# Optimization experiments

Hardware: AMD Instinct MI355X
Metric: run time of the kernel (lower is better)

Reference implementation:

```python
import jax, jax.numpy as jnp
import numpy as np
import math

DIM = 1024
NUM_HEADS = 16
QUANTUM_HEADS = 2
HEAD_DIM = DIM // NUM_HEADS          # 64
TRAD_HEADS = NUM_HEADS - QUANTUM_HEADS  # 14
B, S = 1, 1024
STEPS = 2048
LN_EPS = 1e-5


def setup_inputs() -> dict:
    key = jax.random.key(0)
    ks = jax.random.split(key, 10)
    hd2 = 2 * HEAD_DIM
    return {
        "x": jax.random.normal(ks[0], (B, S, DIM), jnp.float32),
        # to_quantum_state: Linear(head_dim -> 2*head_dim) + LayerNorm + Tanh (shared across quantum heads)
        "qs_W": jax.random.normal(ks[1], (hd2, HEAD_DIM), jnp.float32) / math.sqrt(HEAD_DIM),
        "qs_b": jnp.zeros((hd2,), jnp.float32),
        "ln_g": jnp.ones((hd2,), jnp.float32),
        "ln_b": jnp.zeros((hd2,), jnp.float32),
        # per-quantum-head scalars
        "q_freq": jax.random.normal(ks[2], (QUANTUM_HEADS,), jnp.float32) * 0.02,
        "q_shift": jax.random.normal(ks[3], (QUANTUM_HEADS,), jnp.float32) * 0.02,
        # traditional head projections (no bias)
        "Wq": jax.random.normal(ks[4], (TRAD_HEADS * HEAD_DIM, DIM), jnp.float32) / math.sqrt(DIM),
        "Wk": jax.random.normal(ks[5], (TRAD_HEADS * HEAD_DIM, DIM), jnp.float32) / math.sqrt(DIM),
        "Wv": jax.random.normal(ks[6], (TRAD_HEADS * HEAD_DIM, DIM), jnp.float32) / math.sqrt(DIM),
        # output projection (with bias)
        "Wo": jax.random.normal(ks[7], (DIM, DIM), jnp.float32) / math.sqrt(DIM),
        "bo": jnp.zeros((DIM,), jnp.float32),
    }


def _layernorm(h, g, b):
    mu = jnp.mean(h, axis=-1, keepdims=True)
    var = jnp.mean(jnp.square(h - mu), axis=-1, keepdims=True)
    return (h - mu) * jax.lax.rsqrt(var + LN_EPS) * g + b


def _forward(x, qs_W, qs_b, ln_g, ln_b, q_freq, q_shift, Wq, Wk, Wv, Wo, bo):
    cos_table = jnp.cos(jnp.linspace(0.0, 2.0 * math.pi, STEPS).astype(jnp.float32))
    scale = 1.0 / math.sqrt(HEAD_DIM)
    two_pi = 2.0 * math.pi

    outs = []
    # ---- quantum heads (small fixed loop over structurally distinct heads) ----
    for h in range(QUANTUM_HEADS):
        xh = x[..., h * HEAD_DIM:(h + 1) * HEAD_DIM]          # (B,S,hd)
        qs = jnp.tanh(_layernorm(xh @ qs_W.T + qs_b, ln_g, ln_b))  # (B,S,2hd)
        amp, phase = jnp.split(qs, 2, axis=-1)                 # each (B,S,hd)
        # per (query pos i, key pos j, feature d) phase difference
        pd = (phase[:, :, None, :] - phase[:, None, :, :]) * q_freq[h] + q_shift[h]  # (B,S,S,hd)
        idx = jnp.floor(jnp.mod(pd / two_pi * STEPS, STEPS)).astype(jnp.int32)
        interf = cos_table[idx]                                # lookup-table gather, (B,S,S,hd)
        attn = jnp.einsum('bid,bjd,bijd->bij', amp, amp, interf) * scale
        attn = jax.nn.softmax(attn, axis=-1)
        outs.append(attn @ xh)                                 # (B,S,hd), values are the raw head slice

    # ---- traditional heads: standard multi-head attention ----
    q = (x @ Wq.T).reshape(B, S, TRAD_HEADS, HEAD_DIM)
    k = (x @ Wk.T).reshape(B, S, TRAD_HEADS, HEAD_DIM)
    v = (x @ Wv.T).reshape(B, S, TRAD_HEADS, HEAD_DIM)
    scores = jnp.einsum('bqhd,bkhd->bhqk', q, k) * scale       # (B,Ht,S,S)
    probs = jax.nn.softmax(scores, axis=-1)
    trad = jnp.einsum('bhqk,bkhd->bqhd', probs, v).reshape(B, S, TRAD_HEADS * HEAD_DIM)
    outs.append(trad)

    out = jnp.concatenate(outs, axis=-1)                       # (B,S,DIM)
    return out @ Wo.T + bo


def reference(x, qs_W, qs_b, ln_g, ln_b, q_freq, q_shift, Wq, Wk, Wv, Wo, bo):
    return _forward(x, qs_W, qs_b, ln_g, ln_b, q_freq, q_shift, Wq, Wk, Wv, Wo, bo)
```

## Files before the change

### kernel.cpp

```cpp
#include <hip/hip_runtime.h>
#include <hip/hip_bf16.h>
#include <math.h>

#define DIMX 1024
#define SEQ  1024
#define HD   64
#define QH   2
#define TH   14
#define QKVN 2688
#define LN_EPS 1e-5f
#define NB_F2B 4736
#define NB_QPREP 1024
#define NB_XT 32

typedef __bf16 bf16x8 __attribute__((ext_vector_type(8)));
typedef float  f32x4  __attribute__((ext_vector_type(4)));
typedef unsigned short u16x8 __attribute__((ext_vector_type(8)));

__device__ inline unsigned short f2b_rne(float f) {
  unsigned int u = __float_as_uint(f);
  unsigned int r = (u + 0x7FFF + ((u >> 16) & 1)) >> 16;
  return (unsigned short)r;
}

__device__ inline float waveRedSum(float v) {
  #pragma unroll
  for (int off = 32; off; off >>= 1) v += __shfl_xor(v, off, 64);
  return v;
}

__global__ __launch_bounds__(256) void k_prep(
    const float* __restrict__ x, const float* __restrict__ qsW,
    const float* __restrict__ qsb, const float* __restrict__ lng,
    const float* __restrict__ lnb, const float* __restrict__ qfreq,
    const float* __restrict__ qshift,
    const float* __restrict__ wq, const float* __restrict__ wk,
    const float* __restrict__ wv, const float* __restrict__ wo,
    unsigned short* __restrict__ x_bf, unsigned short* __restrict__ wqkv_bf,
    unsigned short* __restrict__ wo_bf,
    unsigned short* __restrict__ qcs, unsigned short* __restrict__ kcs,
    unsigned short* __restrict__ xt) {
  __shared__ float xrow2[2][HD];
  __shared__ float redm[2][2], redv[2][2];
  __shared__ float qsv2[2][128];
  __shared__ unsigned short ttile[64][72];
  int t = threadIdx.x;
  int bid = blockIdx.x;
  if (bid < NB_F2B) {
    long i = ((long)bid * 256 + t) * 4;
    float4 v;
    unsigned short* dst;
    if (i < 1048576) {
      v = *reinterpret_cast<const float4*>(x + i);
      dst = x_bf + i;
    } else if (i < 3801088) {
      long j = i - 1048576;
      const float* s = (j < 917504) ? wq + j
                     : (j < 1835008) ? wk + (j - 917504)
                                     : wv + (j - 1835008);
      v = *reinterpret_cast<const float4*>(s);
      dst = wqkv_bf + j;
    } else {
      long j = i - 3801088;
      v = *reinterpret_cast<const float4*>(wo + j);
      dst = wo_bf + j;
    }
    ushort4 o;
    o.x = f2b_rne(v.x); o.y = f2b_rne(v.y); o.z = f2b_rne(v.z); o.w = f2b_rne(v.w);
    *reinterpret_cast<ushort4*>(dst) = o;
  } else if (bid < NB_F2B + NB_QPREP) {
    int half = t >> 7, o = t & 127;
    int row = (bid - NB_F2B) * 2 + half;
    int h = row >> 10, i = row & 1023;
    if (o < HD) xrow2[half][o] = x[i * DIMX + h * HD + o];
    __syncthreads();
    float s = qsb[o];
    #pragma unroll
    for (int d = 0; d < HD; d += 4) {
      float4 w = *reinterpret_cast<const float4*>(qsW + o * HD + d);
      float4 xv = *reinterpret_cast<const float4*>(&xrow2[half][d]);
      s += xv.x * w.x + xv.y * w.y + xv.z * w.z + xv.w * w.w;
    }
    int wid = (o >> 6), lane = o & 63;
    float ws = waveRedSum(s);
    if (lane == 0) redm[half][wid] = ws;
    __syncthreads();
    float mu = (redm[half][0] + redm[half][1]) * (1.0f / 128.0f);
    float dv = s - mu;
    float ws2 = waveRedSum(dv * dv);
    if (lane == 0) redv[half][wid] = ws2;
    __syncthreads();
    float var = (redv[half][0] + redv[half][1]) * (1.0f / 128.0f);
    float y = dv * rsqrtf(var + LN_EPS) * lng[o] + lnb[o];
    qsv2[half][o] = tanhf(y);
    __syncthreads();
    float freq = qfreq[h], shift = qshift[h];
    size_t base = ((size_t)h * 1024 + i) * 128;
    if (o < HD) {
      float amp = qsv2[half][o];
      float a = qsv2[half][64 + o] * freq + shift;
      float sn, cs;
      __sincosf(a, &sn, &cs);
      qcs[base + o]      = f2b_rne(amp * cs);
      qcs[base + 64 + o] = f2b_rne(amp * sn);
    } else {
      int d = o - 64;
      float amp = qsv2[half][d];
      float bAng = qsv2[half][64 + d] * freq;
      float sn, cs;
      __sincosf(bAng, &sn, &cs);
      kcs[base + d]      = f2b_rne(amp * cs);
      kcs[base + 64 + d] = f2b_rne(amp * sn);
    }
  } else {
    int b = bid - (NB_F2B + NB_QPREP);
    int h = b >> 4, kv0 = (b & 15) * 64;
    #pragma unroll
    for (int pass = 0; pass < 2; ++pass) {
      int s = pass * 256 + t;
      int r = s >> 3, c8 = (s & 7) * 8;
      const float* src = x + (size_t)(kv0 + r) * DIMX + h * 64 + c8;
      float4 a = *reinterpret_cast<const float4*>(src);
      float4 b4 = *reinterpret_cast<const float4*>(src + 4);
      ushort4 o1, o2;
      o1.x = f2b_rne(a.x);  o1.y = f2b_rne(a.y);  o1.z = f2b_rne(a.z);  o1.w = f2b_rne(a.w);
      o2.x = f2b_rne(b4.x); o2.y = f2b_rne(b4.y); o2.z = f2b_rne(b4.z); o2.w = f2b_rne(b4.w);
      *reinterpret_cast<ushort4*>(&ttile[r][c8]) = o1;
      *reinterpret_cast<ushort4*>(&ttile[r][c8 + 4]) = o2;
    }
    __syncthreads();
    #pragma unroll
    for (int pass = 0; pass < 2; ++pass) {
      int s = pass * 256 + t;
      int d = s >> 3, k8 = (s & 7) * 8;
      u16x8 o;
      #pragma unroll
      for (int j = 0; j < 8; ++j) o[j] = ttile[k8 + j][d];
      *reinterpret_cast<u16x8*>(xt + (size_t)h * 65536 + (size_t)d * 1024 + kv0 + k8) = o;
    }
  }
}

template <int DQK, int NT>
__device__ __forceinline__ void dev_fattn(
    char* smem,
    const unsigned short* __restrict__ Qp, int ldq,
    const unsigned short* __restrict__ Kp, int ldk,
    const unsigned short* __restrict__ Vp,
    int q0, int split, int slot,
    float* __restrict__ pout, float* __restrict__ pml) {
  const int LQ = DQK + 8;
  const int KREG = DQK / 32;
  unsigned short* Qs  = (unsigned short*)smem;
  unsigned short* Ks0 = Qs + 64 * LQ;
  unsigned short* Ks1 = Ks0 + 64 * LQ;
  unsigned short* Vs0 = Ks1 + 64 * LQ;
  unsigned short* Vs1 = Vs0 + 64 * 72;
  unsigned short* Ps  = Vs1 + 64 * 72;
  int kv0 = split * (NT * 64);
  int t = threadIdx.x, lane = t & 63, w = t >> 6;
  int g = lane >> 4, li = lane & 15;

  #pragma unroll
  for (int i = 0; i < DQK / 32; ++i) {
    int s = i * 64 + lane;
    int r = s / (DQK / 8), c8 = (s % (DQK / 8)) * 8;
    u16x8 v = *reinterpret_cast<const u16x8*>(Qp + (size_t)(q0 + w * 16 + r) * ldq + c8);
    *reinterpret_cast<u16x8*>(&Qs[(w * 16 + r) * LQ + c8]) = v;
  }

  u16x8 kreg[KREG], vreg[2];
  auto loadKV = [&](int tile) {
    int j0 = kv0 + tile * 64;
    #pragma unroll
    for (int i = 0; i < KREG; ++i) {
      int s = i * 256 + t;
      int r = s / (DQK / 8), c8 = (s % (DQK / 8)) * 8;
      kreg[i] = *reinterpret_cast<const u16x8*>(Kp + (size_t)(j0 + r) * ldk + c8);
    }
    #pragma unroll
    for (int i = 0; i < 2; ++i) {
      int s = i * 256 + t;
      int d = s >> 3, c8 = (s & 7) * 8;
      vreg[i] = *reinterpret_cast<const u16x8*>(Vp + (size_t)d * 1024 + j0 + c8);
    }
  };
  auto writeKV = [&](int buf) {
    unsigned short* Ksb = buf ? Ks1 : Ks0;
    unsigned short* Vsb = buf ? Vs1 : Vs0;
    #pragma unroll
    for (int i = 0; i < KREG; ++i) {
      int s = i * 256 + t;
      int r = s / (DQK / 8), c8 = (s % (DQK / 8)) * 8;
      *reinterpret_cast<u16x8*>(&Ksb[r * LQ + c8]) = kreg[i];
    }
    #pragma unroll
    for (int i = 0; i < 2; ++i) {
      int s = i * 256 + t;
      int d = s >> 3, c8 = (s & 7) * 8;
      *reinterpret_cast<u16x8*>(&Vsb[d * 72 + c8]) = vreg[i];
    }
  };

  loadKV(0);
  writeKV(0);
  if (NT > 1) loadKV(1);
  __syncthreads();

  f32x4 acc_o[4] = {};
  float mrow[4] = {-1e30f, -1e30f, -1e30f, -1e30f};
  float lrow[4] = {0.f, 0.f, 0.f, 0.f};

  #pragma unroll
  for (int tile = 0; tile < NT; ++tile) {
    int cur = tile & 1;
    unsigned short* Ksc = cur ? Ks1 : Ks0;
    unsigned short* Vsc = cur ? Vs1 : Vs0;
    if (tile < NT - 1) writeKV(cur ^ 1);
    if (tile < NT - 2) loadKV(tile + 2);
    f32x4 s_acc[4] = {};
    #pragma unroll
    for (int kk = 0; kk < DQK / 32; ++kk) {
      bf16x8 aq = *reinterpret_cast<const bf16x8*>(&Qs[(w * 16 + li) * LQ + kk * 32 + g * 8]);
      #pragma unroll
      for (int n = 0; n < 4; ++n) {
        bf16x8 bk = *reinterpret_cast<const bf16x8*>(&Ksc[(n * 16 + li) * LQ + kk * 32 + g * 8]);
        s_acc[n] = __builtin_amdgcn_mfma_f32_16x16x32_bf16(aq, bk, s_acc[n], 0, 0, 0);
      }
    }
    #pragma unroll
    for (int r = 0; r < 4; ++r) {
      float tm = fmaxf(fmaxf(s_acc[0][r], s_acc[1][r]), fmaxf(s_acc[2][r], s_acc[3][r]));
      #pragma unroll
      for (int m = 1; m < 16; m <<= 1) tm = fmaxf(tm, __shfl_xor(tm, m, 64));
      float mn = fmaxf(mrow[r], tm);
      float sf = __expf((mrow[r] - mn) * 0.125f);
      mrow[r] = mn;
      lrow[r] *= sf;
      #pragma unroll
      for (int n = 0; n < 4; ++n) acc_o[n][r] *= sf;
      float rs = 0.f;
      #pragma unroll
      for (int n = 0; n < 4; ++n) {
        float p = __expf((s_acc[n][r] - mn) * 0.125f);
        s_acc[n][r] = p;
        rs += p;
      }
      #pragma unroll
      for (int m = 1; m < 16; m <<= 1) rs += __shfl_xor(rs, m, 64);
      lrow[r] += rs;
    }
    #pragma unroll
    for (int n = 0; n < 4; ++n)
      #pragma unroll
      for (int r = 0; r < 4; ++r)
        Ps[(w * 16 + g * 4 + r) * 72 + n * 16 + li] = f2b_rne(s_acc[n][r]);
    #pragma unroll
    for (int kk = 0; kk < 2; ++kk) {
      bf16x8 ap = *reinterpret_cast<const bf16x8*>(&Ps[(w * 16 + li) * 72 + kk * 32 + g * 8]);
      #pragma unroll
      for (int n = 0; n < 4; ++n) {
        bf16x8 bv = *reinterpret_cast<const bf16x8*>(&Vsc[(n * 16 + li) * 72 + kk * 32 + g * 8]);
        acc_o[n] = __builtin_amdgcn_mfma_f32_16x16x32_bf16(ap, bv, acc_o[n], 0, 0, 0);
      }
    }
    __syncthreads();
  }

  size_t rowbase = (size_t)slot * 1024;
  #pragma unroll
  for (int r = 0; r < 4; ++r) {
    int qr = q0 + w * 16 + g * 4 + r;
    #pragma unroll
    for (int n = 0; n < 4; ++n)
      pout[(rowbase + qr) * 64 + n * 16 + li] = acc_o[n][r];
    if (li == 0) {
      pml[(rowbase + qr) * 2 + 0] = mrow[r];
      pml[(rowbase + qr) * 2 + 1] = lrow[r];
    }
  }
}

__global__ __launch_bounds__(256) void k_fattn_all(
    const unsigned short* __restrict__ qcs, const unsigned short* __restrict__ kcs,
    const unsigned short* __restrict__ xt, const unsigned short* __restrict__ qkv,
    const unsigned short* __restrict__ vt,
    float* __restrict__ pout, float* __restrict__ pml) {
  __shared__ __align__(16) char smem[79872];
  int bid = blockIdx.x;
  if (bid < 256) {
    int qt = bid & 15, h = (bid >> 4) & 1, split = bid >> 5;
    dev_fattn<128, 2>(smem, qcs + (size_t)h * SEQ * 128, 128,
                      kcs + (size_t)h * SEQ * 128, 128,
                      xt + (size_t)h * 65536, qt * 64, split, h * 8 + split, pout, pml);
  } else {
    int b2 = bid - 256;
    int qt = b2 & 15, hs = b2 >> 4;
    int h = hs % 14, split = hs / 14;
    dev_fattn<64, 4>(smem, qkv + h * 64, QKVN,
                     qkv + 896 + h * 64, QKVN,
                     vt + (size_t)h * 65536, qt * 64, split, 16 + h * 4 + split, pout, pml);
  }
}

__global__ __launch_bounds__(256) void k_fmerge(
    const float* __restrict__ pout, const float* __restrict__ pml,
    unsigned short* __restrict__ concat) {
  int rq = blockIdx.x * 4 + (threadIdx.x >> 6);
  int lh = rq >> 10, q = rq & 1023;
  int d = threadIdx.x & 63;
  int s0 = (lh < 2) ? lh * 8 : 16 + (lh - 2) * 4;
  int ns = (lh < 2) ? 8 : 4;
  float m_s[8], l_s[8];
  float M = -1e30f;
  #pragma unroll
  for (int s = 0; s < 8; ++s) {
    if (s < ns) {
      size_t rb = (size_t)(s0 + s) * 1024 + q;
      m_s[s] = pml[rb * 2 + 0];
      l_s[s] = pml[rb * 2 + 1];
      M = fmaxf(M, m_s[s]);
    }
  }
  float num = 0.f, den = 0.f;
  #pragma unroll
  for (int s = 0; s < 8; ++s) {
    if (s < ns) {
      float wgt = __expf((m_s[s] - M) * 0.125f);
      num += wgt * pout[((size_t)(s0 + s) * 1024 + q) * 64 + d];
      den += wgt * l_s[s];
    }
  }
  concat[(size_t)q * DIMX + lh * 64 + d] = f2b_rne(num / den);
}

template <int HAS_BIAS, int BF16_OUT>
__global__ __launch_bounds__(256) void k_gemm64s(
    const unsigned short* __restrict__ A, const unsigned short* __restrict__ B,
    void* __restrict__ Cv, const float* __restrict__ bias,
    unsigned short* __restrict__ vtp,
    int K, int lda, int ldb, int ldc) {
  __shared__ unsigned short As[64 * 64];
  __shared__ unsigned short Bs[64 * 64];
  int t = threadIdx.x, lane = t & 63, w = t >> 6;
  int wr = w >> 1, wc = w & 1;
  int g = lane >> 4, li = lane & 15;
  int mb = blockIdx.y * 64, nb = blockIdx.x * 64;
  int rstg = t >> 3;
  int cswz = (((t & 7) ^ (rstg & 7)) * 8);
  f32x4 acc[2][2] = {};
  for (int kb = 0; kb < K; kb += 64) {
    __syncthreads();
    #pragma unroll
    for (int i = 0; i < 2; ++i) {
      __builtin_amdgcn_global_load_lds(
          (const __attribute__((address_space(1))) unsigned int*)(A + (size_t)(mb + i * 32 + rstg) * lda + kb + cswz),
          (__attribute__((address_space(3))) unsigned int*)(As + i * 2048 + t * 8), 16, 0, 0);
      __builtin_amdgcn_global_load_lds(
          (const __attribute__((address_space(1))) unsigned int*)(B + (size_t)(nb + i * 32 + rstg) * ldb + kb + cswz),
          (__attribute__((address_space(3))) unsigned int*)(Bs + i * 2048 + t * 8), 16, 0, 0);
    }
    __syncthreads();
    #pragma unroll
    for (int kk = 0; kk < 2; ++kk) {
      bf16x8 af[2], bfr[2];
      #pragma unroll
      for (int m = 0; m < 2; ++m) {
        int r = wr * 32 + m * 16 + li;
        int cb = kk * 4 + g;
        af[m] = *reinterpret_cast<const bf16x8*>(&As[r * 64 + ((cb ^ (r & 7)) * 8)]);
      }
      #pragma unroll
      for (int n = 0; n < 2; ++n) {
        int r = wc * 32 + n * 16 + li;
        int cb = kk * 4 + g;
        bfr[n] = *reinterpret_cast<const bf16x8*>(&Bs[r * 64 + ((cb ^ (r & 7)) * 8)]);
      }
      #pragma unroll
      for (int m = 0; m < 2; ++m)
        #pragma unroll
        for (int n = 0; n < 2; ++n)
          acc[m][n] = __builtin_amdgcn_mfma_f32_16x16x32_bf16(af[m], bfr[n], acc[m][n], 0, 0, 0);
    }
  }
  if (vtp != nullptr && nb >= 1792) {
    #pragma unroll
    for (int m = 0; m < 2; ++m) {
      int row0 = mb + wr * 32 + m * 16 + g * 4;
      #pragma unroll
      for (int n = 0; n < 2; ++n) {
        int colrel = nb - 1792 + wc * 32 + n * 16 + li;
        #pragma unroll
        for (int r = 0; r < 4; ++r)
          vtp[(size_t)colrel * 1024 + row0 + r] = f2b_rne(acc[m][n][r]);
      }
    }
    return;
  }
  #pragma unroll
  for (int m = 0; m < 2; ++m) {
    int row0 = mb + wr * 32 + m * 16 + g * 4;
    #pragma unroll
    for (int n = 0; n < 2; ++n) {
      int col = nb + wc * 32 + n * 16 + li;
      float bval = HAS_BIAS ? bias[col] : 0.0f;
      #pragma unroll
      for (int r = 0; r < 4; ++r) {
        size_t idx = (size_t)(row0 + r) * ldc + col;
        if (BF16_OUT) ((unsigned short*)Cv)[idx] = f2b_rne(acc[m][n][r] + bval);
        else          ((float*)Cv)[idx] = acc[m][n][r] + bval;
      }
    }
  }
}

extern "C" void kernel_launch(void* const* d_in, const int* in_sizes, int n_in,
                              void* d_out, int out_size, void* d_ws, size_t ws_size,
                              hipStream_t stream) {
  const float* x      = (const float*)d_in[0];
  const float* qsW    = (const float*)d_in[1];
  const float* qsb    = (const float*)d_in[2];
  const float* lng    = (const float*)d_in[3];
  const float* lnb    = (const float*)d_in[4];
  const float* qfreq  = (const float*)d_in[5];
  const float* qshift = (const float*)d_in[6];
  const float* Wq     = (const float*)d_in[7];
  const float* Wk     = (const float*)d_in[8];
  const float* Wv     = (const float*)d_in[9];
  const float* Wo     = (const float*)d_in[10];
  const float* bo     = (const float*)d_in[11];
  float* out = (float*)d_out;

  char* ws = (char*)d_ws;
  size_t off = 0;
  auto alloc = [&](size_t bytes) { char* p = ws + off; off += (bytes + 255) & ~(size_t)255; return p; };
  unsigned short* x_bf      = (unsigned short*)alloc((size_t)SEQ * DIMX * 2);
  unsigned short* wqkv_bf   = (unsigned short*)alloc((size_t)QKVN * DIMX * 2);
  unsigned short* wo_bf     = (unsigned short*)alloc((size_t)DIMX * DIMX * 2);
  unsigned short* concat_bf = (unsigned short*)alloc((size_t)SEQ * DIMX * 2);
  unsigned short* qkv_bf    = (unsigned short*)alloc((size_t)SEQ * QKVN * 2);
  unsigned short* qcs       = (unsigned short*)alloc((size_t)QH * SEQ * 128 * 2);
  unsigned short* kcs       = (unsigned short*)alloc((size_t)QH * SEQ * 128 * 2);
  unsigned short* vt        = (unsigned short*)alloc((size_t)TH * HD * SEQ * 2);
  unsigned short* xt        = (unsigned short*)alloc((size_t)QH * HD * SEQ * 2);
  float*          pout      = (float*)alloc((size_t)72 * SEQ * 64 * 4);
  float*          pml       = (float*)alloc((size_t)72 * SEQ * 2 * 4);

  k_prep<<<NB_F2B + NB_QPREP + NB_XT, 256, 0, stream>>>(
      x, qsW, qsb, lng, lnb, qfreq, qshift, Wq, Wk, Wv, Wo,
      x_bf, wqkv_bf, wo_bf, qcs, kcs, xt);

  k_gemm64s<0, 1><<<dim3(QKVN / 64, SEQ / 64), 256, 0, stream>>>(
      x_bf, wqkv_bf, qkv_bf, nullptr, vt, DIMX, DIMX, DIMX, QKVN);

  k_fattn_all<<<1152, 256, 0, stream>>>(qcs, kcs, xt, qkv_bf, vt, pout, pml);

  k_fmerge<<<16 * SEQ / 4, 256, 0, stream>>>(pout, pml, concat_bf);

  k_gemm64s<1, 0><<<dim3(DIMX / 64, SEQ / 64), 256, 0, stream>>>(
      concat_bf, wo_bf, out, bo, nullptr, DIMX, DIMX, DIMX, DIMX);
}
```

Before: 80.71 us.

## Split fused attention kernel into per-head-type launches with two-pass softmax and shared K/V buffers

Replaces the single merged attention launch, which reserved a fixed ~78KB shared buffer, with two templated launches sized to each head type. K and V now share the two double buffers. Scores for all KV tiles of a split are kept in registers, so softmax becomes two-pass (max then exp) instead of online rescaling. The aim is lower LDS use per block for more occupancy and removal of the per-tile rescale work, at the cost of more score registers and two serialized launches.

```diff
diff --git a/kernel.cpp b/kernel.cpp
--- a/kernel.cpp
+++ b/kernel.cpp
@@ -142,24 +142,25 @@
 }
 
 template <int DQK, int NT>
-__device__ __forceinline__ void dev_fattn(
-    char* smem,
-    const unsigned short* __restrict__ Qp, int ldq,
-    const unsigned short* __restrict__ Kp, int ldk,
-    const unsigned short* __restrict__ Vp,
-    int q0, int split, int slot,
+__global__ __launch_bounds__(256) void k_fattn2(
+    const unsigned short* __restrict__ Qb, long q_hstep, int ldq,
+    const unsigned short* __restrict__ Kb, long k_hstep, int ldk,
+    const unsigned short* __restrict__ Vtb, long v_hstep, int slot0,
     float* __restrict__ pout, float* __restrict__ pml) {
   const int LQ = DQK + 8;
   const int KREG = DQK / 32;
-  unsigned short* Qs  = (unsigned short*)smem;
-  unsigned short* Ks0 = Qs + 64 * LQ;
-  unsigned short* Ks1 = Ks0 + 64 * LQ;
-  unsigned short* Vs0 = Ks1 + 64 * LQ;
-  unsigned short* Vs1 = Vs0 + 64 * 72;
-  unsigned short* Ps  = Vs1 + 64 * 72;
+  __shared__ unsigned short Qs[64 * (DQK + 8)];
+  __shared__ unsigned short KV0[64 * (DQK + 8)];
+  __shared__ unsigned short KV1[64 * (DQK + 8)];
+  __shared__ unsigned short Ps[64 * 72];
+  int h = blockIdx.y, q0 = blockIdx.x * 64, split = blockIdx.z;
   int kv0 = split * (NT * 64);
+  int slot = slot0 + h * gridDim.z + split;
   int t = threadIdx.x, lane = t & 63, w = t >> 6;
   int g = lane >> 4, li = lane & 15;
+  const unsigned short* Qp = Qb + (size_t)h * q_hstep;
+  const unsigned short* Kp = Kb + (size_t)h * k_hstep;
+  const unsigned short* Vp = Vtb + (size_t)h * v_hstep;
 
   #pragma unroll
   for (int i = 0; i < DQK / 32; ++i) {
@@ -170,7 +171,7 @@
   }
 
   u16x8 kreg[KREG], vreg[2];
-  auto loadKV = [&](int tile) {
+  auto loadK = [&](int tile) {
     int j0 = kv0 + tile * 64;
     #pragma unroll
     for (int i = 0; i < KREG; ++i) {
@@ -178,6 +179,18 @@
       int r = s / (DQK / 8), c8 = (s % (DQK / 8)) * 8;
       kreg[i] = *reinterpret_cast<const u16x8*>(Kp + (size_t)(j0 + r) * ldk + c8);
     }
+  };
+  auto writeK = [&](int buf) {
+    unsigned short* Kd = buf ? KV1 : KV0;
+    #pragma unroll
+    for (int i = 0; i < KREG; ++i) {
+      int s = i * 256 + t;
+      int r = s / (DQK / 8), c8 = (s % (DQK / 8)) * 8;
+      *reinterpret_cast<u16x8*>(&Kd[r * LQ + c8]) = kreg[i];
+    }
+  };
+  auto loadV = [&](int tile) {
+    int j0 = kv0 + tile * 64;
     #pragma unroll
     for (int i = 0; i < 2; ++i) {
       int s = i * 256 + t;
@@ -185,76 +198,76 @@
       vreg[i] = *reinterpret_cast<const u16x8*>(Vp + (size_t)d * 1024 + j0 + c8);
     }
   };
-  auto writeKV = [&](int buf) {
-    unsigned short* Ksb = buf ? Ks1 : Ks0;
-    unsigned short* Vsb = buf ? Vs1 : Vs0;
-    #pragma unroll
-    for (int i = 0; i < KREG; ++i) {
-      int s = i * 256 + t;
-      int r = s / (DQK / 8), c8 = (s % (DQK / 8)) * 8;
-      *reinterpret_cast<u16x8*>(&Ksb[r * LQ + c8]) = kreg[i];
-    }
+  auto writeV = [&](int buf) {
+    unsigned short* Vd = buf ? KV1 : KV0;
     #pragma unroll
     for (int i = 0; i < 2; ++i) {
       int s = i * 256 + t;
       int d = s >> 3, c8 = (s & 7) * 8;
-      *reinterpret_cast<u16x8*>(&Vsb[d * 72 + c8]) = vreg[i];
+      *reinterpret_cast<u16x8*>(&Vd[d * 72 + c8]) = vreg[i];
     }
   };
 
-  loadKV(0);
-  writeKV(0);
-  if (NT > 1) loadKV(1);
+  loadK(0); writeK(0); loadK(1); loadV(0);
   __syncthreads();
 
-  f32x4 acc_o[4] = {};
-  float mrow[4] = {-1e30f, -1e30f, -1e30f, -1e30f};
-  float lrow[4] = {0.f, 0.f, 0.f, 0.f};
+  f32x4 s_all[NT][4] = {};
 
   #pragma unroll
   for (int tile = 0; tile < NT; ++tile) {
-    int cur = tile & 1;
-    unsigned short* Ksc = cur ? Ks1 : Ks0;
-    unsigned short* Vsc = cur ? Vs1 : Vs0;
-    if (tile < NT - 1) writeKV(cur ^ 1);
-    if (tile < NT - 2) loadKV(tile + 2);
-    f32x4 s_acc[4] = {};
+    const unsigned short* Ksc = (tile & 1) ? KV1 : KV0;
+    if (tile < NT - 1) writeK((tile + 1) & 1);
+    if (tile < NT - 2) loadK(tile + 2);
+    if (tile == NT - 1) writeV(0);
     #pragma unroll
     for (int kk = 0; kk < DQK / 32; ++kk) {
       bf16x8 aq = *reinterpret_cast<const bf16x8*>(&Qs[(w * 16 + li) * LQ + kk * 32 + g * 8]);
       #pragma unroll
       for (int n = 0; n < 4; ++n) {
         bf16x8 bk = *reinterpret_cast<const bf16x8*>(&Ksc[(n * 16 + li) * LQ + kk * 32 + g * 8]);
-        s_acc[n] = __builtin_amdgcn_mfma_f32_16x16x32_bf16(aq, bk, s_acc[n], 0, 0, 0);
-      }
-    }
-    #pragma unroll
-    for (int r = 0; r < 4; ++r) {
-      float tm = fmaxf(fmaxf(s_acc[0][r], s_acc[1][r]), fmaxf(s_acc[2][r], s_acc[3][r]));
-      #pragma unroll
-      for (int m = 1; m < 16; m <<= 1) tm = fmaxf(tm, __shfl_xor(tm, m, 64));
-      float mn = fmaxf(mrow[r], tm);
-      float sf = __expf((mrow[r] - mn) * 0.125f);
-      mrow[r] = mn;
-      lrow[r] *= sf;
-      #pragma unroll
-      for (int n = 0; n < 4; ++n) acc_o[n][r] *= sf;
-      float rs = 0.f;
+        s_all[tile][n] = __builtin_amdgcn_mfma_f32_16x16x32_bf16(aq, bk, s_all[tile][n], 0, 0, 0);
+      }
+    }
+    __syncthreads();
+  }
+
+  loadV(1);
+
+  float mrow[4], lrow[4];
+  #pragma unroll
+  for (int r = 0; r < 4; ++r) {
+    float tm = -1e30f;
+    #pragma unroll
+    for (int tile = 0; tile < NT; ++tile)
+      #pragma unroll
+      for (int n = 0; n < 4; ++n) tm = fmaxf(tm, s_all[tile][n][r]);
+    #pragma unroll
+    for (int m = 1; m < 16; m <<= 1) tm = fmaxf(tm, __shfl_xor(tm, m, 64));
+    float rs = 0.f;
+    #pragma unroll
+    for (int tile = 0; tile < NT; ++tile)
       #pragma unroll
       for (int n = 0; n < 4; ++n) {
-        float p = __expf((s_acc[n][r] - mn) * 0.125f);
-        s_acc[n][r] = p;
+        float p = __expf((s_all[tile][n][r] - tm) * 0.125f);
+        s_all[tile][n][r] = p;
         rs += p;
       }
-      #pragma unroll
-      for (int m = 1; m < 16; m <<= 1) rs += __shfl_xor(rs, m, 64);
-      lrow[r] += rs;
-    }
+    #pragma unroll
+    for (int m = 1; m < 16; m <<= 1) rs += __shfl_xor(rs, m, 64);
+    mrow[r] = tm; lrow[r] = rs;
+  }
+
+  f32x4 acc_o[4] = {};
+  #pragma unroll
+  for (int tile = 0; tile < NT; ++tile) {
+    const unsigned short* Vsc = (tile & 1) ? KV1 : KV0;
+    if (tile < NT - 1) writeV((tile + 1) & 1);
+    if (tile < NT - 2) loadV(tile + 2);
     #pragma unroll
     for (int n = 0; n < 4; ++n)
       #pragma unroll
       for (int r = 0; r < 4; ++r)
-        Ps[(w * 16 + g * 4 + r) * 72 + n * 16 + li] = f2b_rne(s_acc[n][r]);
+        Ps[(w * 16 + g * 4 + r) * 72 + n * 16 + li] = f2b_rne(s_all[tile][n][r]);
     #pragma unroll
     for (int kk = 0; kk < 2; ++kk) {
       bf16x8 ap = *reinterpret_cast<const bf16x8*>(&Ps[(w * 16 + li) * 72 + kk * 32 + g * 8]);
@@ -278,28 +291,6 @@
       pml[(rowbase + qr) * 2 + 0] = mrow[r];
       pml[(rowbase + qr) * 2 + 1] = lrow[r];
     }
-  }
-}
-
-__global__ __launch_bounds__(256) void k_fattn_all(
-    const unsigned short* __restrict__ qcs, const unsigned short* __restrict__ kcs,
-    const unsigned short* __restrict__ xt, const unsigned short* __restrict__ qkv,
-    const unsigned short* __restrict__ vt,
-    float* __restrict__ pout, float* __restrict__ pml) {
-  __shared__ __align__(16) char smem[79872];
-  int bid = blockIdx.x;
-  if (bid < 256) {
-    int qt = bid & 15, h = (bid >> 4) & 1, split = bid >> 5;
-    dev_fattn<128, 2>(smem, qcs + (size_t)h * SEQ * 128, 128,
-                      kcs + (size_t)h * SEQ * 128, 128,
-                      xt + (size_t)h * 65536, qt * 64, split, h * 8 + split, pout, pml);
-  } else {
-    int b2 = bid - 256;
-    int qt = b2 & 15, hs = b2 >> 4;
-    int h = hs % 14, split = hs / 14;
-    dev_fattn<64, 4>(smem, qkv + h * 64, QKVN,
-                     qkv + 896 + h * 64, QKVN,
-                     vt + (size_t)h * 65536, qt * 64, split, 16 + h * 4 + split, pout, pml);
   }
 }
 
@@ -453,7 +444,10 @@
   k_gemm64s<0, 1><<<dim3(QKVN / 64, SEQ / 64), 256, 0, stream>>>(
       x_bf, wqkv_bf, qkv_bf, nullptr, vt, DIMX, DIMX, DIMX, QKVN);
 
-  k_fattn_all<<<1152, 256, 0, stream>>>(qcs, kcs, xt, qkv_bf, vt, pout, pml);
+  k_fattn2<64, 4><<<dim3(16, TH, 4), 256, 0, stream>>>(
+      qkv_bf, 64, QKVN, qkv_bf + 896, 64, QKVN, vt, (long)HD * SEQ, 16, pout, pml);
+  k_fattn2<128, 2><<<dim3(16, QH, 8), 256, 0, stream>>>(
+      qcs, (long)SEQ * 128, 128, kcs, (long)SEQ * 128, 128, xt, (long)HD * SEQ, 0, pout, pml);
 
   k_fmerge<<<16 * SEQ / 4, 256, 0, stream>>>(pout, pml, concat_bf);
 
```

Measured after the change: 79.63 us. About the same (-1.3%).
